# Optimization experiments

Hardware: AMD Instinct MI355X
Metric: run time of the kernel (lower is better)

## Reference

```python
import jax, jax.numpy as jnp
import numpy as np

B, T, D_MODEL, HEAD_SIZE = 8, 1024, 1024, 64
BLOCK_SIZE = 1024  # == max_relative_pos


def setup_inputs() -> dict:
    key = jax.random.key(0)
    ks = jax.random.split(key, 7)
    s = 1.0 / np.sqrt(D_MODEL)
    return {
        "x": jax.random.normal(ks[0], (B, T, D_MODEL), dtype=jnp.float32),
        "Wk": jax.random.normal(ks[1], (D_MODEL, HEAD_SIZE), dtype=jnp.float32) * s,
        "bk": jax.random.normal(ks[2], (HEAD_SIZE,), dtype=jnp.float32) * 0.02,
        "Wq": jax.random.normal(ks[3], (D_MODEL, HEAD_SIZE), dtype=jnp.float32) * s,
        "bq": jax.random.normal(ks[4], (HEAD_SIZE,), dtype=jnp.float32) * 0.02,
        "Wv": jax.random.normal(ks[5], (D_MODEL, HEAD_SIZE), dtype=jnp.float32) * s,
        "rel_emb": jax.random.normal(ks[6], (2 * BLOCK_SIZE + 1, HEAD_SIZE), dtype=jnp.float32) * 0.02,
        "mask": 1,
    }


def reference(x, Wk, bk, Wq, bq, Wv, rel_emb, mask):
    Bb, Tt, _ = x.shape
    hs = Wk.shape[1]
    max_rel = (rel_emb.shape[0] - 1) // 2

    k = x @ Wk + bk          # [B,T,hs]
    q = x @ Wq + bq          # [B,T,hs]
    v = x @ Wv               # [B,T,hs]

    pos = jnp.arange(Tt)
    idx = jnp.clip(pos[:, None] - pos[None, :], -max_rel, max_rel) + max_rel
    r = rel_emb[idx]         # [T,T,hs], r[i,j] = emb(clip(i-j))

    # scores[b,i,j] = (q[b,i] + r[i,j]) . (k[b,j] + r[j,i]) / sqrt(hs)
    scale = 1.0 / np.sqrt(hs).astype(np.float32)
    scores = (
        jnp.einsum("bid,bjd->bij", q, k)
        + jnp.einsum("bid,jid->bij", q, r)   # q_i . r[j,i]
        + jnp.einsum("ijd,bjd->bij", r, k)   # r[i,j] . k_j
        + jnp.einsum("ijd,jid->ij", r, r)[None]  # r[i,j] . r[j,i]
    ) * scale

    if mask:  # static Python int -> causal mask, matches tril masked_fill
        causal = jnp.tril(jnp.ones((Tt, Tt), dtype=bool))
        scores = jnp.where(causal, scores, jnp.float32(-jnp.inf))

    w = jax.nn.softmax(scores, axis=-1)  # dropout is identity in eval mode
    return w @ v  # [B,T,hs]
```

## Files before the change

kernel.cpp:

```cpp
#include <hip/hip_runtime.h>
#include <hip/hip_bf16.h>
#include <math.h>


typedef __hip_bfloat16 bf16;
typedef __attribute__((ext_vector_type(8))) short short8;
typedef __attribute__((ext_vector_type(4))) float f32x4;

#define NTILE32 528
#define MFMA16(a, b, c) __builtin_amdgcn_mfma_f32_16x16x32_bf16(a, b, c, 0, 0, 0)

__device__ __forceinline__ float bf2f(bf16 h) { return __bfloat162float(h); }
__device__ __forceinline__ bf16 f2bf(float f) { return __float2bfloat16(f); }
__device__ __forceinline__ short bfs(float f) {
  bf16 h = __float2bfloat16(f);
  return *(short*)&h;
}

union U16 {
  uint4 u;
  short8 s;
};
__device__ __forceinline__ short8 ldfrag(const bf16* p) {
  U16 x;
  x.u = *(const uint4*)p;
  return x.s;
}

__global__ __launch_bounds__(256) void prep_kernel(
    const float* __restrict__ Wk, const float* __restrict__ Wq, const float* __restrict__ Wv,
    const float* __restrict__ E, bf16* __restrict__ WT, bf16* __restrict__ Ep,
    bf16* __restrict__ Erev, float* __restrict__ rrG, float* __restrict__ zeroBase) {
  const int bid = blockIdx.x, t = threadIdx.x;
  if (bid < 768) {
    int idx = bid * 256 + t;
    int sel = idx >> 16, r = idx & 65535;
    int n = r >> 10, kk = r & 1023;
    const float* W = (sel == 0) ? Wk : (sel == 1) ? Wq : Wv;
    WT[idx] = f2bf(W[kk * 64 + n]);
  } else if (bid < 1281) {
    int idx = (bid - 768) * 256 + t;
    if (idx < 2049 * 64) {
      int tt = idx >> 6, d = idx & 63;
      Ep[idx] = f2bf(E[idx]);
      Erev[idx] = f2bf(E[(size_t)(2048 - tt) * 64 + d]);
    }
  } else if (bid < 1537) {
    int dlt = ((bid - 1281) << 2) + (t >> 6);
    int d = t & 63;
    float p = E[(size_t)(1024 + dlt) * 64 + d] * E[(size_t)(1024 - dlt) * 64 + d];
#pragma unroll
    for (int off = 32; off > 0; off >>= 1) p += __shfl_down(p, off);
    if (d == 0) rrG[64 + dlt] = p;
  } else {
    int idx4 = (bid - 1537) * 256 + t;
    if (idx4 < 2048)
      *(float4*)(zeroBase + idx4 * 4) = make_float4(0.f, 0.f, 0.f, 0.f);
  }
}

__global__ __launch_bounds__(256, 2) void qkv_mfma(
    const float* __restrict__ x, const bf16* __restrict__ WT,
    const float* __restrict__ bk, const float* __restrict__ bq,
    bf16* __restrict__ qB, bf16* __restrict__ kB, bf16* __restrict__ vT) {
  const int R0 = blockIdx.x << 4;
  const int t = threadIdx.x;
  const int lane = t & 63, wave = t >> 6;
  const int m = lane & 15, quad = lane >> 4;

  __shared__ float RED[4][16][196];
  __shared__ bf16 VTS[64][24];

  const float* xrow = x + (size_t)(R0 + m) * 1024 + (wave << 8);
  f32x4 acc[3][4];
#pragma unroll
  for (int s = 0; s < 3; ++s)
#pragma unroll
    for (int c = 0; c < 4; ++c) acc[s][c] = (f32x4){0.f, 0.f, 0.f, 0.f};

#pragma unroll
  for (int ks = 0; ks < 8; ++ks) {
    const int k0 = ks * 32 + quad * 8;
    float4 xa = *(const float4*)(xrow + k0);
    float4 xb = *(const float4*)(xrow + k0 + 4);
    short8 a;
    a[0] = bfs(xa.x); a[1] = bfs(xa.y); a[2] = bfs(xa.z); a[3] = bfs(xa.w);
    a[4] = bfs(xb.x); a[5] = bfs(xb.y); a[6] = bfs(xb.z); a[7] = bfs(xb.w);
    const int kg = (wave << 8) + k0;
#pragma unroll
    for (int sel = 0; sel < 3; ++sel)
#pragma unroll
      for (int ct = 0; ct < 4; ++ct) {
        const bf16* bb = WT + ((size_t)(sel * 64 + ct * 16 + m) << 10) + kg;
        acc[sel][ct] = MFMA16(a, ldfrag(bb), acc[sel][ct]);
      }
  }

#pragma unroll
  for (int sel = 0; sel < 3; ++sel)
#pragma unroll
    for (int ct = 0; ct < 4; ++ct)
#pragma unroll
      for (int r = 0; r < 4; ++r)
        RED[wave][quad * 4 + r][sel * 64 + ct * 16 + m] = acc[sel][ct][r];
  __syncthreads();

#pragma unroll
  for (int e = 0; e < 12; ++e) {
    int idx = e * 256 + t;
    int row = idx / 192, c = idx - row * 192;
    float s = RED[0][row][c] + RED[1][row][c] + RED[2][row][c] + RED[3][row][c];
    int sel = c >> 6, col = c & 63;
    size_t grow = (size_t)(R0 + row);
    if (sel == 0) kB[grow * 64 + col] = f2bf(s + bk[col]);
    else if (sel == 1) qB[grow * 64 + col] = f2bf(s + bq[col]);
    else VTS[col][row] = f2bf(s);
  }
  __syncthreads();
  {
    int dd = t >> 2, h = (t & 3) << 2;
    int b = R0 >> 10, tloc = R0 & 1023;
    *(uint2*)(vT + ((size_t)((b << 6) + dd) << 10) + tloc + h) = *(const uint2*)&VTS[dd][h];
  }
}

__global__ __launch_bounds__(256, 3) void flash_mfma(
    const bf16* __restrict__ qB, const bf16* __restrict__ kB, const bf16* __restrict__ vT,
    const bf16* __restrict__ Ep, const bf16* __restrict__ Erev, const float* __restrict__ rrG,
    float* __restrict__ Opart, float* __restrict__ Lacc) {
  const int t = threadIdx.x;
  const int lane = t & 63, wave = t >> 6;
  const int m = lane & 15, quad = lane >> 4;

  const int g = (blockIdx.x << 2) + wave;
  const int b = g / NTILE32;
  const int r0 = g - b * NTILE32;
  int it = (int)((sqrtf(8.f * r0 + 1.f) - 1.f) * 0.5f);
  while ((it + 1) * (it + 2) / 2 <= r0) ++it;
  while (it * (it + 1) / 2 > r0) --it;
  const int jt = r0 - it * (it + 1) / 2;
  const int I0 = it << 5, J0 = jt << 5;
  const int D = I0 - J0, w0 = D - 32;

  __shared__ __align__(16) bf16 M2S[4][32][68];
  __shared__ __align__(16) bf16 M3S[4][32][68];
  bf16 (*M2)[68] = M2S[wave];
  bf16 (*M3)[68] = M3S[wave];
  bf16 (*PS)[40] = (bf16(*)[40]) & M3S[wave][0][0];

  const bf16* qb = qB + ((size_t)((b << 10) + I0) << 6);
  const bf16* kb = kB + ((size_t)((b << 10) + J0) << 6);
  const bf16* erb = Erev + ((size_t)(1024 + w0) << 6);
  const bf16* epb = Ep + ((size_t)(1024 + w0) << 6);

  short8 aq[2][2], kf[2][2];
#pragma unroll
  for (int rt = 0; rt < 2; ++rt)
#pragma unroll
    for (int ks = 0; ks < 2; ++ks) {
      aq[rt][ks] = ldfrag(qb + ((rt * 16 + m) << 6) + ks * 32 + quad * 8);
      kf[rt][ks] = ldfrag(kb + ((rt * 16 + m) << 6) + ks * 32 + quad * 8);
    }
  short8 eb2[4][2], eb3[4][2];
  float rv[4];
#pragma unroll
  for (int ct = 0; ct < 4; ++ct) {
    const bf16* b2p = erb + ((size_t)(ct * 16 + m) << 6) + quad * 8;
    const bf16* b3p = epb + ((size_t)(ct * 16 + m) << 6) + quad * 8;
    eb2[ct][0] = ldfrag(b2p);
    eb2[ct][1] = ldfrag(b2p + 32);
    eb3[ct][0] = ldfrag(b3p);
    eb3[ct][1] = ldfrag(b3p + 32);
    rv[ct] = rrG[64 + w0 + ct * 16 + m];
  }

#pragma unroll
  for (int ct = 0; ct < 4; ++ct) {
#pragma unroll
    for (int rt = 0; rt < 2; ++rt) {
      f32x4 c2 = (f32x4){0.f, 0.f, 0.f, 0.f};
      c2 = MFMA16(aq[rt][0], eb2[ct][0], c2);
      c2 = MFMA16(aq[rt][1], eb2[ct][1], c2);
      f32x4 c3 = (f32x4){0.f, 0.f, 0.f, 0.f};
      c3 = MFMA16(kf[rt][0], eb3[ct][0], c3);
      c3 = MFMA16(kf[rt][1], eb3[ct][1], c3);
#pragma unroll
      for (int r = 0; r < 4; ++r) {
        M2[rt * 16 + quad * 4 + r][ct * 16 + m] = f2bf(c2[r] + rv[ct]);
        M3[rt * 16 + quad * 4 + r][ct * 16 + m] = f2bf(c3[r]);
      }
    }
  }

  f32x4 acc[2][2];
#pragma unroll
  for (int rt = 0; rt < 2; ++rt)
#pragma unroll
    for (int ct = 0; ct < 2; ++ct) {
      f32x4 c = (f32x4){0.f, 0.f, 0.f, 0.f};
      c = MFMA16(aq[rt][0], kf[ct][0], c);
      c = MFMA16(aq[rt][1], kf[ct][1], c);
      acc[rt][ct] = c;
    }

  float sc[2][2][4], lr[2][4];
#pragma unroll
  for (int rt = 0; rt < 2; ++rt)
#pragma unroll
    for (int r = 0; r < 4; ++r) lr[rt][r] = 0.f;
#pragma unroll
  for (int ct = 0; ct < 2; ++ct) {
    const int uj = ct * 16 + m;
#pragma unroll
    for (int rt = 0; rt < 2; ++rt)
#pragma unroll
      for (int r = 0; r < 4; ++r) {
        const int ui = rt * 16 + quad * 4 + r;
        float p = 0.f;
        if (ui - uj + D >= 0) {
          const int wi = ui - uj + 32;
          const float sv = (acc[rt][ct][r] + bf2f(M2[ui][wi]) + bf2f(M3[uj][wi])) * 0.125f;
          p = __expf(sv - 8.0f);
        }
        sc[ct][rt][r] = p;
        lr[rt][r] += p;
      }
  }

  short8 vf[4];
#pragma unroll
  for (int ct = 0; ct < 4; ++ct)
    vf[ct] = ldfrag(vT + ((size_t)(b * 64 + ct * 16 + m) << 10) + J0 + quad * 8);

#pragma unroll
  for (int rt = 0; rt < 2; ++rt)
#pragma unroll
    for (int r = 0; r < 4; ++r) {
#pragma unroll
      for (int off = 1; off < 16; off <<= 1) lr[rt][r] += __shfl_xor(lr[rt][r], off);
    }
  if (m == 0) {
#pragma unroll
    for (int rt = 0; rt < 2; ++rt)
#pragma unroll
      for (int r = 0; r < 4; ++r)
        atomicAdd(&Lacc[(b << 10) + I0 + rt * 16 + quad * 4 + r], lr[rt][r]);
  }

#pragma unroll
  for (int ct = 0; ct < 2; ++ct)
#pragma unroll
    for (int rt = 0; rt < 2; ++rt)
#pragma unroll
      for (int r = 0; r < 4; ++r)
        PS[rt * 16 + quad * 4 + r][ct * 16 + m] = f2bf(sc[ct][rt][r]);

  short8 ap[2];
#pragma unroll
  for (int rt = 0; rt < 2; ++rt) ap[rt] = ldfrag(&PS[rt * 16 + m][quad * 8]);
  float* obp = Opart + ((size_t)(b * NTILE32 + r0) << 11);
#pragma unroll
  for (int ct = 0; ct < 4; ++ct) {
#pragma unroll
    for (int rt = 0; rt < 2; ++rt) {
      f32x4 o = (f32x4){0.f, 0.f, 0.f, 0.f};
      o = MFMA16(ap[rt], vf[ct], o);
#pragma unroll
      for (int r = 0; r < 4; ++r)
        obp[(size_t)((rt * 16 + quad * 4 + r) * 64 + ct * 16 + m)] = o[r];
    }
  }
}

__global__ __launch_bounds__(256) void normalize_kernel(
    const float* __restrict__ Opart, const float* __restrict__ Lacc, float* __restrict__ out) {
  const int idx = blockIdx.x * 256 + threadIdx.x;
  const int b = idx >> 16;
  const int rem = idx & 65535;
  const int i = rem >> 6, d = rem & 63;
  const int it = i >> 5;
  const int base = (it * (it + 1)) >> 1;
  const float* sp = Opart + ((size_t)(b * NTILE32 + base) << 11) + ((i & 31) << 6) + d;
  float s0 = 0.f, s1 = 0.f;
  int jt = 0;
  for (; jt + 1 <= it; jt += 2) {
    s0 += sp[(size_t)jt << 11];
    s1 += sp[(size_t)(jt + 1) << 11];
  }
  if (jt <= it) s0 += sp[(size_t)jt << 11];
  out[idx] = (s0 + s1) / Lacc[idx >> 6];
}

extern "C" void kernel_launch(void* const* d_in, const int* in_sizes, int n_in,
                              void* d_out, int out_size, void* d_ws, size_t ws_size,
                              hipStream_t stream) {
  const float* x = (const float*)d_in[0];
  const float* Wk = (const float*)d_in[1];
  const float* bk = (const float*)d_in[2];
  const float* Wq = (const float*)d_in[3];
  const float* bq = (const float*)d_in[4];
  const float* Wv = (const float*)d_in[5];
  const float* E = (const float*)d_in[6];
  float* out = (float*)d_out;

  float* wsf = (float*)d_ws;
  float* Opart = wsf;
  float* Lacc = wsf + 8650752;
  float* rrG = Lacc + 8192;
  bf16* qB = (bf16*)(rrG + 1152);
  bf16* kB = qB + 524288;
  bf16* vT = kB + 524288;
  bf16* Ep = vT + 524288;
  bf16* Erev = Ep + 131200;
  bf16* WT = Erev + 131200;

  prep_kernel<<<1545, 256, 0, stream>>>(Wk, Wq, Wv, E, WT, Ep, Erev, rrG, Lacc);
  qkv_mfma<<<512, 256, 0, stream>>>(x, WT, bk, bq, qB, kB, vT);
  flash_mfma<<<1056, 256, 0, stream>>>(qB, kB, vT, Ep, Erev, rrG, Opart, Lacc);
  normalize_kernel<<<2048, 256, 0, stream>>>(Opart, Lacc, out);
}
```

Measured before the change: 146.0 us.

## Stage bf16 x tile in LDS and split QKV columns across waves

The QKV projection kernel no longer splits the K dimension across waves and reduces partial sums through a large fp32 shared buffer. Each block now converts its 16 rows of x to bf16 into shared memory once. Each wave then computes three full-K 16-column output tiles, so no cross-wave reduction is needed. The smaller LDS footprint allows a higher launch-bounds occupancy hint (4 blocks). In exchange, each wave runs a longer serial K loop of 32 steps with fewer independent accumulators per wave.

```diff
diff --git a/kernel.cpp b/kernel.cpp
--- a/kernel.cpp
+++ b/kernel.cpp
@@ -59,7 +59,7 @@
   }
 }
 
-__global__ __launch_bounds__(256, 2) void qkv_mfma(
+__global__ __launch_bounds__(256, 4) void qkv_mfma(
     const float* __restrict__ x, const bf16* __restrict__ WT,
     const float* __restrict__ bk, const float* __restrict__ bq,
     bf16* __restrict__ qB, bf16* __restrict__ kB, bf16* __restrict__ vT) {
@@ -68,53 +68,52 @@
   const int lane = t & 63, wave = t >> 6;
   const int m = lane & 15, quad = lane >> 4;
 
-  __shared__ float RED[4][16][196];
+  __shared__ __align__(16) bf16 XS[16][1032];
   __shared__ bf16 VTS[64][24];
 
-  const float* xrow = x + (size_t)(R0 + m) * 1024 + (wave << 8);
-  f32x4 acc[3][4];
-#pragma unroll
-  for (int s = 0; s < 3; ++s)
-#pragma unroll
-    for (int c = 0; c < 4; ++c) acc[s][c] = (f32x4){0.f, 0.f, 0.f, 0.f};
-
-#pragma unroll
-  for (int ks = 0; ks < 8; ++ks) {
-    const int k0 = ks * 32 + quad * 8;
-    float4 xa = *(const float4*)(xrow + k0);
-    float4 xb = *(const float4*)(xrow + k0 + 4);
-    short8 a;
-    a[0] = bfs(xa.x); a[1] = bfs(xa.y); a[2] = bfs(xa.z); a[3] = bfs(xa.w);
-    a[4] = bfs(xb.x); a[5] = bfs(xb.y); a[6] = bfs(xb.z); a[7] = bfs(xb.w);
-    const int kg = (wave << 8) + k0;
-#pragma unroll
-    for (int sel = 0; sel < 3; ++sel)
-#pragma unroll
-      for (int ct = 0; ct < 4; ++ct) {
-        const bf16* bb = WT + ((size_t)(sel * 64 + ct * 16 + m) << 10) + kg;
-        acc[sel][ct] = MFMA16(a, ldfrag(bb), acc[sel][ct]);
-      }
-  }
-
-#pragma unroll
-  for (int sel = 0; sel < 3; ++sel)
-#pragma unroll
-    for (int ct = 0; ct < 4; ++ct)
-#pragma unroll
-      for (int r = 0; r < 4; ++r)
-        RED[wave][quad * 4 + r][sel * 64 + ct * 16 + m] = acc[sel][ct][r];
+#pragma unroll
+  for (int i = 0; i < 16; ++i) {
+    const float4 xa = *(const float4*)(x + (size_t)(R0 + i) * 1024 + t * 4);
+    union { ushort4 h; uint2 u; } pk;
+    bf16 h0 = f2bf(xa.x), h1 = f2bf(xa.y), h2 = f2bf(xa.z), h3 = f2bf(xa.w);
+    pk.h.x = *(unsigned short*)&h0;
+    pk.h.y = *(unsigned short*)&h1;
+    pk.h.z = *(unsigned short*)&h2;
+    pk.h.w = *(unsigned short*)&h3;
+    *(uint2*)&XS[i][t * 4] = pk.u;
+  }
   __syncthreads();
 
-#pragma unroll
-  for (int e = 0; e < 12; ++e) {
-    int idx = e * 256 + t;
-    int row = idx / 192, c = idx - row * 192;
-    float s = RED[0][row][c] + RED[1][row][c] + RED[2][row][c] + RED[3][row][c];
-    int sel = c >> 6, col = c & 63;
-    size_t grow = (size_t)(R0 + row);
-    if (sel == 0) kB[grow * 64 + col] = f2bf(s + bk[col]);
-    else if (sel == 1) qB[grow * 64 + col] = f2bf(s + bq[col]);
-    else VTS[col][row] = f2bf(s);
+  f32x4 acc[3];
+#pragma unroll
+  for (int j = 0; j < 3; ++j) acc[j] = (f32x4){0.f, 0.f, 0.f, 0.f};
+  const int g0 = wave * 3;
+  const bf16* wb[3];
+#pragma unroll
+  for (int j = 0; j < 3; ++j) {
+    const int gg = g0 + j, sel = gg >> 2, ctl = gg & 3;
+    wb[j] = WT + ((size_t)(sel * 64 + ctl * 16 + m) << 10) + quad * 8;
+  }
+#pragma unroll
+  for (int ks = 0; ks < 32; ++ks) {
+    const short8 a = ldfrag(&XS[m][ks * 32 + quad * 8]);
+#pragma unroll
+    for (int j = 0; j < 3; ++j)
+      acc[j] = MFMA16(a, ldfrag(wb[j] + ks * 32), acc[j]);
+  }
+
+#pragma unroll
+  for (int j = 0; j < 3; ++j) {
+    const int gg = g0 + j, sel = gg >> 2, ctl = gg & 3;
+    const int col = ctl * 16 + m;
+#pragma unroll
+    for (int r = 0; r < 4; ++r) {
+      const float s = acc[j][r];
+      const size_t grow = (size_t)(R0 + quad * 4 + r);
+      if (sel == 0) kB[grow * 64 + col] = f2bf(s + bk[col]);
+      else if (sel == 1) qB[grow * 64 + col] = f2bf(s + bq[col]);
+      else VTS[col][quad * 4 + r] = f2bf(s);
+    }
   }
   __syncthreads();
   {
```

Result: no change. 145.7 us (-0.2%).
